# Optimization experiments

Hardware: AMD Instinct MI355X
Metric: run time of the kernel (lower is better)

## Reference

```python
import jax, jax.numpy as jnp
import numpy as np

POOL_RATIO = 0.25
ROUTING_NUM = 3
B, N, D, H = 32, 2048, 512, 512


def setup_inputs() -> dict:
    key = jax.random.key(0)
    k_x, k_adj, k_w = jax.random.split(key, 3)
    x = jax.random.normal(k_x, (B, N, D), dtype=jnp.float32)
    # variable node counts per graph; row 0 uses all N nodes so max_cluster is static
    rng = np.random.default_rng(0)
    lens = np.full(B, N, dtype=np.int64)
    lens[1:] = rng.integers(N // 2, N + 1, size=B - 1)
    mask_np = (np.arange(N)[None, :] < lens[:, None])  # [B,N] bool
    mask = jnp.asarray(mask_np)
    # sparse-ish random adjacency, zeroed outside the node mask
    adj = (jax.random.uniform(k_adj, (B, N, N)) < 0.01).astype(jnp.float32)
    m = mask.astype(jnp.float32)
    adj = adj * m[:, None, :] * m[:, :, None]
    W = jax.random.normal(k_w, (D, H), dtype=jnp.float32) * 0.02
    b = jnp.zeros((H,), dtype=jnp.float32)
    return {"x": x, "adj": adj, "W": W, "b": b, "mask": mask}


def masked_softmax(s, m):
    # m: bool broadcastable to s; masked entries -> exactly 0 probability
    s = jnp.where(m, s, jnp.float32(-1e9))
    return jax.nn.softmax(s, axis=-1) * m


def squash(s):
    # squash along last (feature) dim, as in torch sum(dim=2) on [B,C,H]
    mag_sq = jnp.sum(s * s, axis=-1, keepdims=True)
    mag = jnp.sqrt(mag_sq)
    return mag_sq / (1.0 + mag_sq) * (s / mag)


def reference(x, adj, W, b, mask):
    fmask = mask.astype(x.dtype)
    node_num = fmask.sum(axis=1)                               # [B]
    cluster_num = jnp.floor(node_num * POOL_RATIO).astype(jnp.int32)
    max_cluster = int(x.shape[1] * POOL_RATIO)                 # static (row 0 has N nodes)
    cmask = jnp.arange(max_cluster)[None, :] < cluster_num[:, None]  # [B,C] bool
    cm = cmask[:, None, :]                                     # [B,1,C]
    # embed: dense GCN layer  z = relu(adj @ x @ W + b)  -> [B,N,H]
    z = jax.nn.relu(jnp.einsum('bnm,bmd,dh->bnh', adj, x, W) + b)
    s = jax.random.normal(jax.random.key(42), (x.shape[0], x.shape[1], max_cluster), dtype=x.dtype)
    for _ in range(ROUTING_NUM):
        s = masked_softmax(s, cm)                              # [B,N,C]
        xnext = squash(jnp.einsum('bnc,bnh->bch', s, z))       # [B,C,H]
        s = s + jnp.einsum('bnh,bch->bnc', z, xnext)           # routing update
    return masked_softmax(s, cm)
```

## Files before the change

kernel.cpp:

```cpp
#include <hip/hip_runtime.h>
#include <cstdint>
#include <cstddef>

#define NB 32
#define NN 2048
#define ND 512
#define NH 512
#define NC 512
#define ROWS (NB*NN)

typedef __attribute__((ext_vector_type(8))) short short8v;
typedef __attribute__((ext_vector_type(4))) float f32x4;

#define MFMA16(a,b,c) __builtin_amdgcn_mfma_f32_16x16x32_bf16((a),(b),(c),0,0,0)

typedef const __attribute__((address_space(1))) unsigned int* gas_t;
typedef __attribute__((address_space(3))) unsigned int* las_t;

__device__ __forceinline__ void gload16(const void* g, void* l){
  __builtin_amdgcn_global_load_lds((gas_t)g, (las_t)l, 16, 0, 0);
}

__device__ __forceinline__ void fsplit(float v, unsigned short& h, unsigned short& l){
  unsigned u = __float_as_uint(v);
  unsigned hb = (u + 0x7FFFu + ((u>>16)&1u)) >> 16;
  float hf = __uint_as_float(hb<<16);
  float r = v - hf;
  unsigned ur = __float_as_uint(r);
  l = (unsigned short)((ur + 0x7FFFu + ((ur>>16)&1u)) >> 16);
  h = (unsigned short)hb;
}

__device__ __forceinline__ unsigned rotl32(unsigned x, int d){ return (x<<d)|(x>>(32-d)); }

__device__ __forceinline__ unsigned threefry_xor(unsigned k0, unsigned k1, unsigned c0, unsigned c1){
  unsigned ks2 = 0x1BD11BDAu ^ k0 ^ k1;
  unsigned x0 = c0 + k0, x1 = c1 + k1;
#define TF_RND(r) { x0 += x1; x1 = rotl32(x1,(r)); x1 ^= x0; }
  TF_RND(13) TF_RND(15) TF_RND(26) TF_RND(6)
  x0 += k1;  x1 += ks2 + 1u;
  TF_RND(17) TF_RND(29) TF_RND(16) TF_RND(24)
  x0 += ks2; x1 += k0 + 2u;
  TF_RND(13) TF_RND(15) TF_RND(26) TF_RND(6)
  x0 += k0;  x1 += k1 + 3u;
  TF_RND(17) TF_RND(29) TF_RND(16) TF_RND(24)
  x0 += k1;  x1 += ks2 + 4u;
  TF_RND(13) TF_RND(15) TF_RND(26) TF_RND(6)
  x0 += ks2; x1 += k0 + 5u;
#undef TF_RND
  return x0 ^ x1;
}

__device__ __forceinline__ float bits_to_normal(unsigned bits){
  float f = __uint_as_float((bits >> 9) | 0x3f800000u) - 1.0f;
  const float lo = -0.99999994f;
  float u = fmaxf(lo, fmaf(f, 2.0f, lo));
  float w = -log1pf(-(u*u));
  float p;
  if (w < 5.0f){
    w -= 2.5f;
    p =            2.81022636e-08f;
    p = fmaf(p, w, 3.43273939e-07f);
    p = fmaf(p, w, -3.5233877e-06f);
    p = fmaf(p, w, -4.39150654e-06f);
    p = fmaf(p, w, 0.00021858087f);
    p = fmaf(p, w, -0.00125372503f);
    p = fmaf(p, w, -0.00417768164f);
    p = fmaf(p, w, 0.246640727f);
    p = fmaf(p, w, 1.50140941f);
  } else {
    w = sqrtf(w) - 3.0f;
    p =            -0.000200214257f;
    p = fmaf(p, w, 0.000100950558f);
    p = fmaf(p, w, 0.00134934322f);
    p = fmaf(p, w, -0.00367342844f);
    p = fmaf(p, w, 0.00573950773f);
    p = fmaf(p, w, -0.0076224613f);
    p = fmaf(p, w, 0.00943887047f);
    p = fmaf(p, w, 1.00167406f);
    p = fmaf(p, w, 2.83297682f);
  }
  return 1.4142135623730951f * (p * u);
}

__global__ void __launch_bounds__(256) rng_kernel(float* __restrict__ s){
  unsigned i = blockIdx.x * 256u + threadIdx.x;
  s[i] = bits_to_normal(threefry_xor(0u, 42u, 0u, i));
}

__global__ void __launch_bounds__(256) counts_kernel(const unsigned char* __restrict__ mraw,
                                                     int* __restrict__ cnum,
                                                     int* __restrict__ lenbuf){
  __shared__ int red[256];
  int b = blockIdx.x, tid = threadIdx.x;
  unsigned char b0 = mraw[0], b1 = mraw[1];
  int cnt = 0;
  if (b0 == 1 && b1 == 1){
    const unsigned char* p = mraw + (size_t)b * NN;
    for (int i = tid; i < NN; i += 256) cnt += (p[i] != 0);
  } else if (b0 == 1){
    const int* p = (const int*)mraw + (size_t)b * NN;
    for (int i = tid; i < NN; i += 256) cnt += (p[i] != 0);
  } else {
    const float* p = (const float*)mraw + (size_t)b * NN;
    for (int i = tid; i < NN; i += 256) cnt += (p[i] != 0.0f);
  }
  red[tid] = cnt; __syncthreads();
  for (int off = 128; off; off >>= 1){ if (tid < off) red[tid] += red[tid+off]; __syncthreads(); }
  if (tid == 0){ cnum[b] = red[0] >> 2; lenbuf[b] = red[0]; }
}

__global__ void __launch_bounds__(256) spmm_kernel(const float* __restrict__ adj,
                                                   const float* __restrict__ x,
                                                   unsigned short* __restrict__ yh,
                                                   unsigned short* __restrict__ yl,
                                                   const int* __restrict__ lenbuf){
  __shared__ int   idxs[NN];
  __shared__ float vals[NN];
  __shared__ int   scan[256];
  int row = blockIdx.x;
  int b = row >> 11;
  int n = row & 2047;
  int tid = threadIdx.x;
  size_t base = (size_t)row * ND;
  if (n >= lenbuf[b]){
    yh[base+tid]=0; yl[base+tid]=0; yh[base+tid+256]=0; yl[base+tid+256]=0;
    return;
  }
  const float* arow = adj + (size_t)row * NN;
  float v[8];
  *(float4*)&v[0] = *(const float4*)(arow + tid*8);
  *(float4*)&v[4] = *(const float4*)(arow + tid*8 + 4);
  int lc = 0;
  #pragma unroll
  for (int j=0;j<8;j++) lc += (v[j] != 0.0f);
  scan[tid] = lc; __syncthreads();
  for (int off=1; off<256; off<<=1){
    int t = (tid >= off) ? scan[tid-off] : 0;
    __syncthreads();
    scan[tid] += t;
    __syncthreads();
  }
  int pos = scan[tid] - lc;
  int total = scan[255];
  #pragma unroll
  for (int j=0;j<8;j++){
    if (v[j] != 0.0f){ idxs[pos] = tid*8 + j; vals[pos] = v[j]; pos++; }
  }
  __syncthreads();
  float acc0 = 0.f, acc1 = 0.f;
  const float* xb = x + (size_t)b * NN * ND;
  for (int j=0;j<total;j++){
    int m = idxs[j]; float a = vals[j];
    acc0 = fmaf(a, xb[(size_t)m*ND + tid      ], acc0);
    acc1 = fmaf(a, xb[(size_t)m*ND + tid + 256], acc1);
  }
  unsigned short h,l;
  fsplit(acc0,h,l); yh[base+tid]=h;     yl[base+tid]=l;
  fsplit(acc1,h,l); yh[base+tid+256]=h; yl[base+tid+256]=l;
}

__global__ void __launch_bounds__(256) wsplit_kernel(const float* __restrict__ W,
                                                     unsigned short* __restrict__ WTh,
                                                     unsigned short* __restrict__ WTl){
  __shared__ float t[32][33];
  int bx = blockIdx.x, by = blockIdx.y;
  int x = threadIdx.x & 31, y = threadIdx.x >> 5;
  for (int yy=y; yy<32; yy+=8) t[yy][x] = W[(size_t)(bx*32+yy)*512 + by*32 + x];
  __syncthreads();
  for (int yy=y; yy<32; yy+=8){
    float v = t[x][yy];
    unsigned short h,l; fsplit(v,h,l);
    size_t idx = (size_t)(by*32+yy)*512 + bx*32 + x;
    WTh[idx]=h; WTl[idx]=l;
  }
}

template<bool SPLIT, bool WF32>
__global__ void __launch_bounds__(256) softmax_kernel(float* __restrict__ s,
                                                      unsigned short* __restrict__ sh,
                                                      unsigned short* __restrict__ sl,
                                                      const int* __restrict__ cnum){
  int row  = blockIdx.x*4 + (threadIdx.x >> 6);
  int lane = threadIdx.x & 63;
  int b = row >> 11;
  int Kc = cnum[b];
  float* p = s + (size_t)row * NC;
  float4 v0 = *(const float4*)(p + lane*4);
  float4 v1 = *(const float4*)(p + lane*4 + 256);
  float e[8] = {v0.x,v0.y,v0.z,v0.w,v1.x,v1.y,v1.z,v1.w};
  float m = -3.0e38f;
  #pragma unroll
  for (int j=0;j<8;j++){
    int c = (j<4) ? lane*4 + j : lane*4 + 252 + j;
    if (c < Kc) m = fmaxf(m, e[j]);
  }
  #pragma unroll
  for (int off=32; off; off>>=1) m = fmaxf(m, __shfl_xor(m, off, 64));
  float r[8]; float sum = 0.f;
  #pragma unroll
  for (int j=0;j<8;j++){
    int c = (j<4) ? lane*4 + j : lane*4 + 252 + j;
    r[j] = (c < Kc) ? expf(e[j] - m) : 0.0f;
    sum += r[j];
  }
  #pragma unroll
  for (int off=32; off; off>>=1) sum += __shfl_xor(sum, off, 64);
  float inv = 1.0f / sum;
  #pragma unroll
  for (int j=0;j<8;j++) r[j] *= inv;
  if constexpr (WF32){
    *(float4*)(p + lane*4)       = make_float4(r[0],r[1],r[2],r[3]);
    *(float4*)(p + lane*4 + 256) = make_float4(r[4],r[5],r[6],r[7]);
  }
  if constexpr (SPLIT){
    unsigned long long ph=0, pl=0, qh=0, ql=0;
    #pragma unroll
    for (int j=0;j<4;j++){
      unsigned short h,l;
      fsplit(r[j],h,l);
      ph |= (unsigned long long)h << (16*j);  pl |= (unsigned long long)l << (16*j);
      fsplit(r[4+j],h,l);
      qh |= (unsigned long long)h << (16*j);  ql |= (unsigned long long)l << (16*j);
    }
    size_t base = (size_t)row * NC + lane*4;
    *(unsigned long long*)(sh + base)       = ph;
    *(unsigned long long*)(sl + base)       = pl;
    *(unsigned long long*)(sh + base + 256) = qh;
    *(unsigned long long*)(sl + base + 256) = ql;
  }
}

template<int EPI, bool SWZ>
__global__ void __launch_bounds__(512,2) gemm256_kernel(
    const unsigned short* __restrict__ Ah, const unsigned short* __restrict__ Al,
    const unsigned short* __restrict__ Bh, const unsigned short* __restrict__ Bl,
    unsigned short* __restrict__ OutH, unsigned short* __restrict__ OutL,
    float* __restrict__ Cf, const unsigned short* __restrict__ S2h,
    const unsigned short* __restrict__ S2l,
    const float* __restrict__ bias, const float* __restrict__ scale,
    const int* __restrict__ lenbuf, const int* __restrict__ cnumbuf,
    int K, long sA, long sB, long sC)
{
  __shared__ __align__(16) unsigned char smem[131072];
  int bx, by, bz;
  if constexpr (SWZ){
    int flat = blockIdx.x;
    int f2 = (flat & 7)*64 + (flat >> 3);
    bz = f2 >> 4; int rem = f2 & 15; bx = rem >> 1; by = rem & 1;
  } else { bx = blockIdx.x; by = blockIdx.y; bz = blockIdx.z; }
  Ah += (size_t)bz*sA; Al += (size_t)bz*sA;
  Bh += (size_t)bz*sB; Bl += (size_t)bz*sB;
  if constexpr (EPI==2){
    Cf += (size_t)bz*sC; S2h += (size_t)bz*sC; S2l += (size_t)bz*sC;
    scale += (size_t)bz*NC;
  }
  int m0 = bx*256, n0 = by*256;
  int lim_m, lim_n;
  if constexpr (EPI==1){
    lim_m = lenbuf[m0 >> 11] - (m0 & 2047);
    lim_n = 256;
  } else {
    lim_m = lenbuf[bz] - m0;
    lim_n = cnumbuf[bz] - n0;
  }
  int tid = threadIdx.x;
  int l = tid & 63, wid = tid >> 6;
  int wr = wid >> 2, wc = wid & 3;
  int lr = l & 15, lk = l >> 4;

  bool liA[8]; bool liB[4];
  int offA[8], offB[4];
  #pragma unroll
  for (int i=0;i<8;i++){
    int ra = wr*128 + i*16 + lr;
    offA[i] = ra*64 + ((lk ^ ((ra>>1)&3))<<4);
    liA[i] = (wr*128 + i*16) < lim_m;
  }
  #pragma unroll
  for (int j=0;j<4;j++){
    int rb = wc*64 + j*16 + lr;
    offB[j] = rb*64 + ((lk ^ ((rb>>1)&3))<<4);
    liB[j] = (wc*64 + j*16) < lim_n;
  }

  int srow = tid >> 2;
  int gslot = (tid & 3) ^ ((srow>>1)&3);
  const unsigned short* gA0 = Ah + (size_t)(m0 +       srow)*512 + gslot*8;
  const unsigned short* gA1 = Ah + (size_t)(m0 + 128 + srow)*512 + gslot*8;
  const unsigned short* gA2 = Al + (size_t)(m0 +       srow)*512 + gslot*8;
  const unsigned short* gA3 = Al + (size_t)(m0 + 128 + srow)*512 + gslot*8;
  const unsigned short* gB0 = Bh + (size_t)(n0 +       srow)*512 + gslot*8;
  const unsigned short* gB1 = Bh + (size_t)(n0 + 128 + srow)*512 + gslot*8;
  const unsigned short* gB2 = Bl + (size_t)(n0 +       srow)*512 + gslot*8;
  const unsigned short* gB3 = Bl + (size_t)(n0 + 128 + srow)*512 + gslot*8;

  f32x4 acc[8][4] = {};

#define STAGE256(buf, k0) { \
    unsigned char* db = smem + (buf)*65536 + wid*1024; \
    gload16(gA0 + (k0), db);          gload16(gA1 + (k0), db + 8192); \
    gload16(gA2 + (k0), db + 16384);  gload16(gA3 + (k0), db + 24576); \
    gload16(gB0 + (k0), db + 32768);  gload16(gB1 + (k0), db + 40960); \
    gload16(gB2 + (k0), db + 49152);  gload16(gB3 + (k0), db + 57344); }

  STAGE256(0, 0)
  __syncthreads();
  int KT = K >> 5;
  for (int t = 0; t < KT; ++t){
    if (t+1 < KT) STAGE256((t+1)&1, (t+1)*32)
    const unsigned char* base = smem + (t&1)*65536;
    short8v ah[8], bh[4], bl[4];
    #pragma unroll
    for (int i=0;i<8;i++) if (liA[i]) ah[i] = *(const short8v*)(base + offA[i]);
    #pragma unroll
    for (int j=0;j<4;j++) if (liB[j]){
      bh[j] = *(const short8v*)(base + 32768 + offB[j]);
      bl[j] = *(const short8v*)(base + 49152 + offB[j]);
    }
    #pragma unroll
    for (int i=0;i<8;i++) if (liA[i])
      #pragma unroll
      for (int j=0;j<4;j++) if (liB[j]) acc[i][j] = MFMA16(ah[i], bh[j], acc[i][j]);
    #pragma unroll
    for (int i=0;i<8;i++) if (liA[i])
      #pragma unroll
      for (int j=0;j<4;j++) if (liB[j]) acc[i][j] = MFMA16(ah[i], bl[j], acc[i][j]);
    #pragma unroll
    for (int i=0;i<8;i++) if (liA[i]){
      short8v al = *(const short8v*)(base + 16384 + offA[i]);
      #pragma unroll
      for (int j=0;j<4;j++) if (liB[j]) acc[i][j] = MFMA16(al, bh[j], acc[i][j]);
    }
    __syncthreads();
  }
#undef STAGE256

  float aux[4];
  #pragma unroll
  for (int j=0;j<4;j++){
    int gcol = n0 + wc*64 + j*16 + lr;
    if constexpr (EPI==1) aux[j] = bias[gcol];
    if constexpr (EPI==2) aux[j] = scale[gcol];
  }
  #pragma unroll
  for (int i=0;i<8;i++){
    #pragma unroll
    for (int r=0;r<4;r++){
      int grow = m0 + wr*128 + i*16 + lk*4 + r;
      size_t rowb = (size_t)grow*512 + n0 + wc*64 + lr;
      #pragma unroll
      for (int j=0;j<4;j++){
        float v = acc[i][j][r];
        if constexpr (EPI==1){
          v = fmaxf(v + aux[j], 0.f);
          unsigned short h,lo2; fsplit(v,h,lo2);
          OutH[rowb + j*16] = h; OutL[rowb + j*16] = lo2;
        } else {
          unsigned hh = S2h[rowb + j*16], ll = S2l[rowb + j*16];
          float s2 = __uint_as_float(hh<<16) + __uint_as_float(ll<<16);
          Cf[rowb + j*16] = s2 + aux[j]*v;
        }
      }
    }
  }
}

__global__ void __launch_bounds__(512,2) gemmT256_kernel(
    const unsigned short* __restrict__ Ah, const unsigned short* __restrict__ Al,
    const unsigned short* __restrict__ Bh, const unsigned short* __restrict__ Bl,
    unsigned short* __restrict__ OutH, unsigned short* __restrict__ OutL,
    float* __restrict__ parts, const int* __restrict__ lenbuf,
    const int* __restrict__ cnumbuf)
{
  __shared__ __align__(16) unsigned char smem[98304];
  int flat = blockIdx.x;
  int f2 = (flat & 7)*32 + (flat >> 3);
  int bz = f2 >> 3; int rem = f2 & 7; int bx = rem & 1; int by = rem >> 1;
  size_t boff = (size_t)bz * NN * 512;
  Ah += boff; Al += boff; Bh += boff; Bl += boff;
  int m0 = bx*256, n0 = by*128;
  int KT = (lenbuf[bz] + 31) >> 5;
  int limc = cnumbuf[bz] - m0;
  int tid = threadIdx.x;
  int l = tid & 63, wid = tid >> 6;
  int wr = wid >> 2, wc = wid & 3;
  int lr = l & 15, lk = l >> 4;

  bool liA[8];
  int offA[8], offB[2];
  #pragma unroll
  for (int i=0;i<8;i++){
    int ra = wr*128 + i*16 + lr;
    offA[i] = ra*64 + ((lk ^ ((ra>>1)&3) ^ ((ra>>3)&3))<<4);
    liA[i] = (wr*128 + i*16) < limc;
  }
  #pragma unroll
  for (int j=0;j<2;j++){
    int rb = wc*32 + j*16 + lr;
    offB[j] = rb*64 + ((lk ^ ((rb>>1)&3) ^ ((rb>>3)&3))<<4);
  }

  int np  = tid & 15;
  int seg = tid >> 4;
  f32x4 acc[8][2] = {};

  short8v ra0h, ra1h, ra0l, ra1l, rb0h, rb1h, rb0l, rb1l;
  int have_b = (tid < 256);

#define TLOAD(k0) { \
    size_t ga = (size_t)((k0) + 2*np)*512 + m0 + seg*8; \
    ra0h = *(const short8v*)(Ah + ga); ra1h = *(const short8v*)(Ah + ga + 512); \
    ra0l = *(const short8v*)(Al + ga); ra1l = *(const short8v*)(Al + ga + 512); \
    if (have_b){ \
      size_t gb = (size_t)((k0) + 2*np)*512 + n0 + seg*8; \
      rb0h = *(const short8v*)(Bh + gb); rb1h = *(const short8v*)(Bh + gb + 512); \
      rb0l = *(const short8v*)(Bl + gb); rb1l = *(const short8v*)(Bl + gb + 512); } }

#define TWRITE(buf) { \
    unsigned char* bb = smem + (buf)*49152; \
    _Pragma("unroll") \
    for (int k=0;k<8;k++){ \
      int c = seg*8 + k; \
      int ps = (np>>2) ^ ((c>>1)&3) ^ ((c>>3)&3); \
      int byo = c*64 + ps*16 + (np&3)*4; \
      *(unsigned int*)(bb + byo)         = (unsigned int)(unsigned short)ra0h[k] | ((unsigned int)(unsigned short)ra1h[k]<<16); \
      *(unsigned int*)(bb + 16384 + byo) = (unsigned int)(unsigned short)ra0l[k] | ((unsigned int)(unsigned short)ra1l[k]<<16); \
      if (have_b){ \
        *(unsigned int*)(bb + 32768 + byo) = (unsigned int)(unsigned short)rb0h[k] | ((unsigned int)(unsigned short)rb1h[k]<<16); \
        *(unsigned int*)(bb + 40960 + byo) = (unsigned int)(unsigned short)rb0l[k] | ((unsigned int)(unsigned short)rb1l[k]<<16); } } }

  TLOAD(0)
  TWRITE(0)
  __syncthreads();
  for (int t = 0; t < KT; ++t){
    int more = (t+1 < KT);
    if (more) TLOAD((t+1)*32)
    const unsigned char* base = smem + (t&1)*49152;
    short8v ah[8], bh[2], bl[2];
    #pragma unroll
    for (int i=0;i<8;i++) if (liA[i]) ah[i] = *(const short8v*)(base + offA[i]);
    #pragma unroll
    for (int j=0;j<2;j++){
      bh[j] = *(const short8v*)(base + 32768 + offB[j]);
      bl[j] = *(const short8v*)(base + 40960 + offB[j]);
    }
    #pragma unroll
    for (int i=0;i<8;i++) if (liA[i])
      #pragma unroll
      for (int j=0;j<2;j++) acc[i][j] = MFMA16(ah[i], bh[j], acc[i][j]);
    #pragma unroll
    for (int i=0;i<8;i++) if (liA[i])
      #pragma unroll
      for (int j=0;j<2;j++) acc[i][j] = MFMA16(ah[i], bl[j], acc[i][j]);
    #pragma unroll
    for (int i=0;i<8;i++) if (liA[i]){
      short8v al = *(const short8v*)(base + 16384 + offA[i]);
      #pragma unroll
      for (int j=0;j<2;j++) acc[i][j] = MFMA16(al, bh[j], acc[i][j]);
    }
    if (more) TWRITE((t+1)&1)
    __syncthreads();
  }
#undef TLOAD
#undef TWRITE

  #pragma unroll
  for (int i=0;i<8;i++){
    #pragma unroll
    for (int r=0;r<4;r++){
      int grow = m0 + wr*128 + i*16 + lk*4 + r;
      float p = 0.f;
      size_t rowb = (size_t)bz*NC*NH + (size_t)grow*512 + n0 + wc*32 + lr;
      #pragma unroll
      for (int j=0;j<2;j++){
        float v = acc[i][j][r];
        p = fmaf(v,v,p);
        unsigned short h,lo2; fsplit(v,h,lo2);
        OutH[rowb + j*16] = h; OutL[rowb + j*16] = lo2;
      }
      p += __shfl_xor(p, 1, 64);
      p += __shfl_xor(p, 2, 64);
      p += __shfl_xor(p, 4, 64);
      p += __shfl_xor(p, 8, 64);
      if (lr == 0) parts[(((size_t)bz*NC) + grow)*16 + by*4 + wc] = p;
    }
  }
}

__global__ void __launch_bounds__(512) scale_kernel(const float* __restrict__ parts,
                                                    float* __restrict__ scale){
  int b = blockIdx.x, c = threadIdx.x;
  const float* p = parts + ((size_t)b*NC + c)*16;
  float m2 = 0.f;
  #pragma unroll
  for (int j=0;j<16;j++) m2 += p[j];
  float sc = 0.0f;
  if (m2 > 0.0f) sc = (m2/(1.0f+m2)) / sqrtf(m2);
  scale[(size_t)b*NC + c] = sc;
}

extern "C" void kernel_launch(void* const* d_in, const int* in_sizes, int n_in,
                              void* d_out, int out_size, void* d_ws, size_t ws_size,
                              hipStream_t stream) {
  const float* x    = (const float*)d_in[0];
  const float* adj  = (const float*)d_in[1];
  const float* W    = (const float*)d_in[2];
  const float* bias = (const float*)d_in[3];
  const unsigned char* mask = (const unsigned char*)d_in[4];
  float* out = (float*)d_out;
  char* ws = (char*)d_ws;

  unsigned short* zh   = (unsigned short*)(ws);
  unsigned short* zl   = (unsigned short*)(ws + 67108864);
  unsigned short* sth  = (unsigned short*)(ws + 134217728);
  unsigned short* stl  = (unsigned short*)(ws + 201326592);
  unsigned short* xnh  = (unsigned short*)(ws + 268435456);
  unsigned short* xnl  = (unsigned short*)(ws + 285212672);
  unsigned short* WTh  = (unsigned short*)(ws + 301989888);
  unsigned short* WTl  = (unsigned short*)(ws + 302514176);
  float* parts         = (float*)(ws + 303038464);
  float* scalebuf      = (float*)(ws + 304087040);
  int*   cnum          = (int*)(ws + 304152576);
  int*   lenbuf        = (int*)(ws + 304152704);
  unsigned short* yh = sth;
  unsigned short* yl = stl;

  counts_kernel<<<NB, 256, 0, stream>>>(mask, cnum, lenbuf);
  wsplit_kernel<<<dim3(16,16), 256, 0, stream>>>(W, WTh, WTl);
  spmm_kernel<<<ROWS, 256, 0, stream>>>(adj, x, yh, yl, lenbuf);
  gemm256_kernel<1,false><<<dim3(256,2,1), 512, 0, stream>>>(
      yh, yl, WTh, WTl, zh, zl, nullptr, nullptr, nullptr, bias, nullptr,
      lenbuf, cnum, ND, 0, 0, 0);
  rng_kernel<<<(ROWS*NC)/256, 256, 0, stream>>>(out);

  for (int it = 0; it < 3; ++it){
    softmax_kernel<true,false><<<ROWS/4, 256, 0, stream>>>(out, sth, stl, cnum);
    gemmT256_kernel<<<256, 512, 0, stream>>>(
        sth, stl, zh, zl, xnh, xnl, parts, lenbuf, cnum);
    scale_kernel<<<NB, 512, 0, stream>>>(parts, scalebuf);
    gemm256_kernel<2,true><<<512, 512, 0, stream>>>(
        zh, zl, xnh, xnl, nullptr, nullptr, out, sth, stl, nullptr, scalebuf,
        lenbuf, cnum, NH, (long)NN*NH, (long)NC*NH, (long)NN*NC);
  }
  softmax_kernel<false,true><<<ROWS/4, 256, 0, stream>>>(out, nullptr, nullptr, cnum);
}
```

Measured before the change: 1.467 ms.

## Single-buffer gemm256 LDS and drop masked-tile skipping

Halves the gemm256 shared-memory tile from double to single buffer. Each K step now waits on outstanding loads, copies all fragments into registers, syncs, issues the next tile's global-to-LDS loads, then runs the MFMAs at raised wave priority. The per-row/column validity predicates derived from node and cluster counts are removed, so every tile does full MFMA work even where the graph is padded. The smaller LDS footprint may allow higher occupancy, at the cost of more registers held for fragments and wasted compute on masked regions.

```diff
diff --git a/kernel.cpp b/kernel.cpp
--- a/kernel.cpp
+++ b/kernel.cpp
@@ -239,10 +239,9 @@
     float* __restrict__ Cf, const unsigned short* __restrict__ S2h,
     const unsigned short* __restrict__ S2l,
     const float* __restrict__ bias, const float* __restrict__ scale,
-    const int* __restrict__ lenbuf, const int* __restrict__ cnumbuf,
     int K, long sA, long sB, long sC)
 {
-  __shared__ __align__(16) unsigned char smem[131072];
+  __shared__ __align__(16) unsigned char smem[65536];
   int bx, by, bz;
   if constexpr (SWZ){
     int flat = blockIdx.x;
@@ -256,32 +255,21 @@
     scale += (size_t)bz*NC;
   }
   int m0 = bx*256, n0 = by*256;
-  int lim_m, lim_n;
-  if constexpr (EPI==1){
-    lim_m = lenbuf[m0 >> 11] - (m0 & 2047);
-    lim_n = 256;
-  } else {
-    lim_m = lenbuf[bz] - m0;
-    lim_n = cnumbuf[bz] - n0;
-  }
   int tid = threadIdx.x;
   int l = tid & 63, wid = tid >> 6;
   int wr = wid >> 2, wc = wid & 3;
   int lr = l & 15, lk = l >> 4;
 
-  bool liA[8]; bool liB[4];
   int offA[8], offB[4];
   #pragma unroll
   for (int i=0;i<8;i++){
     int ra = wr*128 + i*16 + lr;
     offA[i] = ra*64 + ((lk ^ ((ra>>1)&3))<<4);
-    liA[i] = (wr*128 + i*16) < lim_m;
   }
   #pragma unroll
   for (int j=0;j<4;j++){
     int rb = wc*64 + j*16 + lr;
     offB[j] = rb*64 + ((lk ^ ((rb>>1)&3))<<4);
-    liB[j] = (wc*64 + j*16) < lim_n;
   }
 
   int srow = tid >> 2;
@@ -297,44 +285,47 @@
 
   f32x4 acc[8][4] = {};
 
-#define STAGE256(buf, k0) { \
-    unsigned char* db = smem + (buf)*65536 + wid*1024; \
+#define STAGE1(k0) { \
+    unsigned char* db = smem + wid*1024; \
     gload16(gA0 + (k0), db);          gload16(gA1 + (k0), db + 8192); \
     gload16(gA2 + (k0), db + 16384);  gload16(gA3 + (k0), db + 24576); \
     gload16(gB0 + (k0), db + 32768);  gload16(gB1 + (k0), db + 40960); \
     gload16(gB2 + (k0), db + 49152);  gload16(gB3 + (k0), db + 57344); }
 
-  STAGE256(0, 0)
-  __syncthreads();
+  STAGE1(0)
   int KT = K >> 5;
   for (int t = 0; t < KT; ++t){
-    if (t+1 < KT) STAGE256((t+1)&1, (t+1)*32)
-    const unsigned char* base = smem + (t&1)*65536;
-    short8v ah[8], bh[4], bl[4];
-    #pragma unroll
-    for (int i=0;i<8;i++) if (liA[i]) ah[i] = *(const short8v*)(base + offA[i]);
-    #pragma unroll
-    for (int j=0;j<4;j++) if (liB[j]){
-      bh[j] = *(const short8v*)(base + 32768 + offB[j]);
-      bl[j] = *(const short8v*)(base + 49152 + offB[j]);
-    }
-    #pragma unroll
-    for (int i=0;i<8;i++) if (liA[i])
-      #pragma unroll
-      for (int j=0;j<4;j++) if (liB[j]) acc[i][j] = MFMA16(ah[i], bh[j], acc[i][j]);
-    #pragma unroll
-    for (int i=0;i<8;i++) if (liA[i])
-      #pragma unroll
-      for (int j=0;j<4;j++) if (liB[j]) acc[i][j] = MFMA16(ah[i], bl[j], acc[i][j]);
-    #pragma unroll
-    for (int i=0;i<8;i++) if (liA[i]){
-      short8v al = *(const short8v*)(base + 16384 + offA[i]);
-      #pragma unroll
-      for (int j=0;j<4;j++) if (liB[j]) acc[i][j] = MFMA16(al, bh[j], acc[i][j]);
-    }
+    asm volatile("s_waitcnt vmcnt(0)" ::: "memory");
     __syncthreads();
-  }
-#undef STAGE256
+    short8v ah[8], al[8], bh[4], bl[4];
+    #pragma unroll
+    for (int i=0;i<8;i++){
+      ah[i] = *(const short8v*)(smem + offA[i]);
+      al[i] = *(const short8v*)(smem + 16384 + offA[i]);
+    }
+    #pragma unroll
+    for (int j=0;j<4;j++){
+      bh[j] = *(const short8v*)(smem + 32768 + offB[j]);
+      bl[j] = *(const short8v*)(smem + 49152 + offB[j]);
+    }
+    __syncthreads();
+    if (t+1 < KT) STAGE1((t+1)*32)
+    __builtin_amdgcn_s_setprio(1);
+    #pragma unroll
+    for (int i=0;i<8;i++)
+      #pragma unroll
+      for (int j=0;j<4;j++) acc[i][j] = MFMA16(ah[i], bh[j], acc[i][j]);
+    #pragma unroll
+    for (int i=0;i<8;i++)
+      #pragma unroll
+      for (int j=0;j<4;j++) acc[i][j] = MFMA16(ah[i], bl[j], acc[i][j]);
+    #pragma unroll
+    for (int i=0;i<8;i++)
+      #pragma unroll
+      for (int j=0;j<4;j++) acc[i][j] = MFMA16(al[i], bh[j], acc[i][j]);
+    __builtin_amdgcn_s_setprio(0);
+  }
+#undef STAGE1
 
   float aux[4];
   #pragma unroll
@@ -531,7 +522,7 @@
   spmm_kernel<<<ROWS, 256, 0, stream>>>(adj, x, yh, yl, lenbuf);
   gemm256_kernel<1,false><<<dim3(256,2,1), 512, 0, stream>>>(
       yh, yl, WTh, WTl, zh, zl, nullptr, nullptr, nullptr, bias, nullptr,
-      lenbuf, cnum, ND, 0, 0, 0);
+      ND, 0, 0, 0);
   rng_kernel<<<(ROWS*NC)/256, 256, 0, stream>>>(out);
 
   for (int it = 0; it < 3; ++it){
@@ -541,7 +532,7 @@
     scale_kernel<<<NB, 512, 0, stream>>>(parts, scalebuf);
     gemm256_kernel<2,true><<<512, 512, 0, stream>>>(
         zh, zl, xnh, xnl, nullptr, nullptr, out, sth, stl, nullptr, scalebuf,
-        lenbuf, cnum, NH, (long)NN*NH, (long)NC*NH, (long)NN*NC);
+        NH, (long)NN*NH, (long)NC*NH, (long)NN*NC);
   }
   softmax_kernel<false,true><<<ROWS/4, 256, 0, stream>>>(out, nullptr, nullptr, cnum);
 }
```

Measured after the change: 1.417 ms. 1.04x faster.
